# Performance work log

Measured on AMD Instinct MI355X. Metric: run time of the kernel, lower is better.

## Reference

```python
import jax, jax.numpy as jnp
import numpy as np

B, N, D = 32, 4096, 256
NC, NTPC, NVPT, NS = 16, 8, 4, 16
NT = NC * NTPC          # 128 type codes
NV = NT * NVPT          # 512 variant codes
THRESH = 0.1            # code_sparsity


def setup_inputs() -> dict:
    key = jax.random.key(0)
    ks = jax.random.split(key, 24)
    rn = lambda k, s, sc=0.02: jax.random.normal(k, s, jnp.float32) * sc
    return {
        "X": jax.random.normal(ks[0], (B, N, D), jnp.float32),
        "positions": jax.random.normal(ks[1], (B, N, D), jnp.float32),
        "mask": jnp.ones((B, N), jnp.bool_),
        "category_codes": rn(ks[2], (NC, D)),
        "type_codes": rn(ks[3], (NT, D)),
        "variant_codes": rn(ks[4], (NV, D)),
        "spatial_codes": rn(ks[5], (NS, D)),
        "log_tau": jnp.zeros((1,), jnp.float32),
        "Wk": rn(ks[6], (D, D)), "bk": jnp.zeros((D,), jnp.float32),
        "Wcat": rn(ks[7], (D, D)), "bcat": jnp.zeros((D,), jnp.float32),
        "Wtype": rn(ks[8], (D, D)), "btype": jnp.zeros((D,), jnp.float32),
        "Wvar": rn(ks[9], (D, D)), "bvar": jnp.zeros((D,), jnp.float32),
        "Wsp": rn(ks[10], (D, D)), "bsp": jnp.zeros((D,), jnp.float32),
        "Wg1": rn(ks[11], (D, 2 * D)), "bg1": jnp.zeros((D,), jnp.float32),
        "Wg2": rn(ks[12], (D, D)), "bg2": jnp.zeros((D,), jnp.float32),
        "Wo": rn(ks[13], (D, D)), "bo": jnp.zeros((D,), jnp.float32),
        "ln_g": jnp.ones((D,), jnp.float32), "ln_b": jnp.zeros((D,), jnp.float32),
        "level_weights": jnp.ones((4,), jnp.float32) / 4.0,
    }


def _sparsify(w, thr):
    w = jnp.where(w > thr, w, 0.0)
    return w / (w.sum(-1, keepdims=True) + 1e-8)


def reference(X, positions, mask, category_codes, type_codes, variant_codes,
              spatial_codes, log_tau, Wk, bk, Wcat, bcat, Wtype, btype,
              Wvar, bvar, Wsp, bsp, Wg1, bg1, Wg2, bg2, Wo, bo, ln_g, ln_b,
              level_weights):
    d = X.shape[-1]
    tau = jnp.clip(jnp.exp(log_tau) + 0.1, 0.1, 2.0)  # (1,)
    mv = jnp.finfo(X.dtype).min / 2
    K = X @ Wk.T + bk  # (B,N,d)

    def level(codes, Wq, bq):
        Q = codes @ Wq.T + bq                                    # (M,d)
        attn = jnp.einsum('md,bnd->bmn', Q, K) / jnp.sqrt(jnp.float32(d))
        attn = jnp.where(mask[:, None, :], attn, mv)
        attn = jnp.clip(attn, -50.0, 50.0)
        G = jnp.nan_to_num(jax.nn.softmax(attn, axis=-1))
        H = jnp.einsum('bmn,bnd->bmd', G, X)                     # (B,M,d)
        w_raw = jnp.linalg.norm(H, axis=-1) / tau                # (B,M)
        return H, w_raw

    # level 0: category
    H_cat, w_cat_raw = level(category_codes, Wcat, bcat)
    w_cat_sparse = _sparsify(jax.nn.softmax(w_cat_raw, -1), THRESH)
    # level 1: type (gated by category)
    H_type, w_type_raw = level(type_codes, Wtype, btype)
    w_type_g = (w_type_raw.reshape(-1, NC, NTPC) * w_cat_sparse[:, :, None]).reshape(-1, NT)
    w_type_sparse = _sparsify(jax.nn.softmax(w_type_g, -1), THRESH / 2)
    # level 2: variant (gated by type)
    H_var, w_var_raw = level(variant_codes, Wvar, bvar)
    w_type_exp = jnp.repeat(w_type_sparse, NVPT, axis=-1)        # (B,NV)
    w_var_sparse = _sparsify(jax.nn.softmax(w_var_raw * w_type_exp, -1), THRESH / 4)
    # spatial (independent)
    H_sp, w_sp_raw = level(spatial_codes, Wsp, bsp)
    w_sp_sparse = _sparsify(jax.nn.softmax(w_sp_raw, -1), THRESH)

    z_cat = jnp.einsum('bm,bmd->bd', w_cat_sparse, H_cat)
    z_type = jnp.einsum('bm,bmd->bd', w_type_sparse, H_type)
    z_var = jnp.einsum('bm,bmd->bd', w_var_sparse, H_var)
    z_sp = jnp.einsum('bm,bmd->bd', w_sp_sparse, H_sp)

    lw = jax.nn.softmax(level_weights)
    z = lw[0] * z_cat + lw[1] * z_type + lw[2] * z_var + lw[3] * z_sp

    # position gate: masked mean-pooled positions -> sigmoid gate
    m = mask.astype(X.dtype)
    pos_pool = (positions * m[:, :, None]).sum(1) / (m.sum(1, keepdims=True) + 1e-8)
    h = jax.nn.gelu(jnp.concatenate([z, pos_pool], -1) @ Wg1.T + bg1, approximate=False)
    gate = jax.nn.sigmoid(h @ Wg2.T + bg2)
    z = z * gate

    # out_proj: Linear + LayerNorm
    y = z @ Wo.T + bo
    mu = y.mean(-1, keepdims=True)
    var = ((y - mu) ** 2).mean(-1, keepdims=True)
    y = (y - mu) / jnp.sqrt(var + 1e-5) * ln_g + ln_b
    return y
```

## Files before the change

### kernel.cpp

```cpp
#include <hip/hip_runtime.h>

typedef unsigned short u16;
typedef short v8s __attribute__((ext_vector_type(8)));
typedef float v4f __attribute__((ext_vector_type(4)));

union U16x8 { uint4 u4; v8s s8; u16 us[8]; };

__device__ __forceinline__ u16 f2bf(float x) {
  unsigned int u = __float_as_uint(x);
  u += 0x7fffu + ((u >> 16) & 1u);
  return (u16)(u >> 16);
}

#define GLOBAL_AS __attribute__((address_space(1)))
#define LDS_AS __attribute__((address_space(3)))
__device__ __forceinline__ void async16(const void* g, void* l) {
  __builtin_amdgcn_global_load_lds((const GLOBAL_AS unsigned int*)g,
                                   (LDS_AS unsigned int*)l, 16, 0, 0);
}

#define BB 32
#define NN 4096
#define DD 256
#define M_TOT 672
#define M_PAD 704
#define CHUNK_B 16

__global__ void kz_zero(float* __restrict__ p, int n) {
  int i = blockIdx.x * 256 + threadIdx.x;
  if (i < n) p[i] = 0.f;
}

__global__ void k0_q(const float* __restrict__ cat, const float* __restrict__ typ,
                     const float* __restrict__ var, const float* __restrict__ spc,
                     const float* __restrict__ Wcat, const float* __restrict__ bcat,
                     const float* __restrict__ Wtype, const float* __restrict__ btype,
                     const float* __restrict__ Wvar, const float* __restrict__ bvar,
                     const float* __restrict__ Wsp, const float* __restrict__ bsp,
                     float* __restrict__ Qall) {
  __shared__ float cl[DD];
  const int m = blockIdx.x, tid = threadIdx.x;
  const float* codes = nullptr; const float* W = nullptr; const float* bia = nullptr; int r = 0;
  if (m < 16)       { codes = cat; r = m;       W = Wcat;  bia = bcat; }
  else if (m < 144) { codes = typ; r = m - 16;  W = Wtype; bia = btype; }
  else if (m < 656) { codes = var; r = m - 144; W = Wvar;  bia = bvar; }
  else if (m < 672) { codes = spc; r = m - 656; W = Wsp;   bia = bsp; }
  cl[tid] = (m < M_TOT) ? codes[r * DD + tid] : 0.f;
  __syncthreads();
  if (m < M_TOT) {
    float acc = bia[tid];
    const float4* w4 = (const float4*)(W + (size_t)tid * DD);
    const float4* c4 = (const float4*)cl;
    #pragma unroll 8
    for (int k = 0; k < 64; ++k) {
      float4 a = c4[k], b = w4[k];
      acc += a.x * b.x + a.y * b.y + a.z * b.z + a.w * b.w;
    }
    Qall[m * DD + tid] = acc;
  } else {
    Qall[m * DD + tid] = 0.f;
  }
}

__global__ void k1_qp(const float* __restrict__ Qall, const float* __restrict__ Wk,
                      const float* __restrict__ bk, u16* __restrict__ Qp,
                      float* __restrict__ qbw) {
  __shared__ float ql[DD];
  __shared__ float red[4];
  const int m = blockIdx.x, tid = threadIdx.x;
  ql[tid] = Qall[m * DD + tid];
  __syncthreads();
  float acc = 0.f;
  for (int j = 0; j < DD; ++j) acc += ql[j] * Wk[(size_t)j * DD + tid];
  Qp[m * DD + tid] = f2bf(acc);
  float p = ql[tid] * bk[tid];
  #pragma unroll
  for (int off = 32; off > 0; off >>= 1) p += __shfl_down(p, off, 64);
  if ((tid & 63) == 0) red[tid >> 6] = p;
  __syncthreads();
  if (tid == 0) qbw[m] = red[0] + red[1] + red[2] + red[3];
}

__global__ void k2_cast(const float* __restrict__ X, u16* __restrict__ Xb,
                        u16* __restrict__ XbT) {
  __shared__ u16 tl[64][72];
  const int n0 = blockIdx.x * 64, d0 = blockIdx.y * 64, b = blockIdx.z;
  const int tid = threadIdx.x;
  const int nl = tid >> 4, d4 = tid & 15;
  #pragma unroll
  for (int rr = 0; rr < 4; ++rr) {
    const int n = n0 + nl + rr * 16;
    float4 v = *(const float4*)(X + ((size_t)b * NN + n) * DD + d0 + d4 * 4);
    ushort4 h;
    h.x = f2bf(v.x); h.y = f2bf(v.y); h.z = f2bf(v.z); h.w = f2bf(v.w);
    *(ushort4*)(Xb + ((size_t)b * NN + n) * DD + d0 + d4 * 4) = h;
    *(ushort4*)(&tl[nl + rr * 16][d4 * 4]) = h;
  }
  __syncthreads();
  const int dl = tid >> 4, n4 = tid & 15;
  #pragma unroll
  for (int rr = 0; rr < 4; ++rr) {
    const int d = dl + rr * 16;
    ushort4 h;
    h.x = tl[n4 * 4 + 0][d]; h.y = tl[n4 * 4 + 1][d];
    h.z = tl[n4 * 4 + 2][d]; h.w = tl[n4 * 4 + 3][d];
    *(ushort4*)(XbT + ((size_t)b * DD + d0 + d) * NN + n0 + n4 * 4) = h;
  }
}

__global__ __launch_bounds__(256, 2) void p1_scores(
    const u16* __restrict__ Xb, const u16* __restrict__ Qp,
    const float* __restrict__ qbw, const unsigned char* __restrict__ mask,
    u16* __restrict__ P, float* __restrict__ sums, int b0) {
  __shared__ u16 sA[128 * 64];
  __shared__ u16 sB[128 * 64];
  const int tid = threadIdx.x;
  const int lane = tid & 63, w = tid >> 6;
  const int q = lane >> 4, c16 = lane & 15;
  const int n0 = blockIdx.x * 128, m0 = blockIdx.y * 128;
  const int b = b0 + blockIdx.z;
  const int wm = (w >> 1) * 64, wn = (w & 1) * 64;

  float qv[4][4];
  unsigned char mk[4];
  #pragma unroll
  for (int mi = 0; mi < 4; ++mi)
    #pragma unroll
    for (int r = 0; r < 4; ++r) {
      int row = m0 + wm + mi * 16 + q * 4 + r;
      qv[mi][r] = qbw[row < M_PAD ? row : M_PAD - 1];
    }
  #pragma unroll
  for (int ni = 0; ni < 4; ++ni)
    mk[ni] = mask[(size_t)b * NN + n0 + wn + ni * 16 + c16];

  v4f acc[4][4];
  #pragma unroll
  for (int mi = 0; mi < 4; ++mi)
    #pragma unroll
    for (int ni = 0; ni < 4; ++ni) acc[mi][ni] = (v4f){0.f, 0.f, 0.f, 0.f};

  const u16* Xbase = Xb + (size_t)b * NN * DD;
  for (int ks = 0; ks < 4; ++ks) {
    __syncthreads();
    #pragma unroll
    for (int i = 0; i < 4; ++i) {
      const int c = i * 256 + tid;
      const int row = c >> 3, kc = (c & 7) * 8;
      int gm = m0 + row; gm = gm < M_PAD ? gm : M_PAD - 1;
      async16(Qp + (size_t)gm * DD + ks * 64 + kc, sA + c * 8);
      async16(Xbase + (size_t)(n0 + row) * DD + ks * 64 + kc, sB + c * 8);
    }
    __syncthreads();
    #pragma unroll
    for (int kk = 0; kk < 2; ++kk) {
      v8s af[4], bf[4];
      #pragma unroll
      for (int mi = 0; mi < 4; ++mi) {
        U16x8 u; u.u4 = *(const uint4*)(sA + (wm + mi * 16 + c16) * 64 + kk * 32 + q * 8);
        af[mi] = u.s8;
      }
      #pragma unroll
      for (int ni = 0; ni < 4; ++ni) {
        U16x8 u; u.u4 = *(const uint4*)(sB + (wn + ni * 16 + c16) * 64 + kk * 32 + q * 8);
        bf[ni] = u.s8;
      }
      #pragma unroll
      for (int mi = 0; mi < 4; ++mi)
        #pragma unroll
        for (int ni = 0; ni < 4; ++ni)
          acc[mi][ni] = __builtin_amdgcn_mfma_f32_16x16x32_bf16(af[mi], bf[ni], acc[mi][ni], 0, 0, 0);
    }
  }

  float rs[4][4];
  #pragma unroll
  for (int mi = 0; mi < 4; ++mi)
    #pragma unroll
    for (int r = 0; r < 4; ++r) rs[mi][r] = 0.f;

  #pragma unroll
  for (int mi = 0; mi < 4; ++mi) {
    #pragma unroll
    for (int ni = 0; ni < 4; ++ni) {
      #pragma unroll
      for (int r = 0; r < 4; ++r) {
        float s = (acc[mi][ni][r] + qv[mi][r]) * 0.0625f;
        s = fminf(fmaxf(s, -50.f), 50.f);
        s = mk[ni] ? s : -50.f;
        float p = __expf(s);
        rs[mi][r] += p;
        const int row = m0 + wm + mi * 16 + q * 4 + r;
        if (row < M_TOT)
          P[((size_t)(b - b0) * M_TOT + row) * NN + n0 + wn + ni * 16 + c16] = f2bf(p);
      }
    }
  }
  #pragma unroll
  for (int mi = 0; mi < 4; ++mi) {
    #pragma unroll
    for (int r = 0; r < 4; ++r) {
      float v = rs[mi][r];
      v += __shfl_xor(v, 1, 64);
      v += __shfl_xor(v, 2, 64);
      v += __shfl_xor(v, 4, 64);
      v += __shfl_xor(v, 8, 64);
      const int row = m0 + wm + mi * 16 + q * 4 + r;
      if (c16 == 0 && row < M_TOT)
        atomicAdd(&sums[(size_t)b * M_PAD + row], v);
    }
  }
}

__global__ __launch_bounds__(256, 4) void p2_h(
    const u16* __restrict__ P, const u16* __restrict__ XbT,
    const float* __restrict__ sums, float* __restrict__ Hws,
    float* __restrict__ nrm, int b0) {
  __shared__ u16 sA[64 * 64];
  __shared__ u16 sB[128 * 64];
  const int tid = threadIdx.x;
  const int lane = tid & 63, w = tid >> 6;
  const int q = lane >> 4, c16 = lane & 15;
  const int d0 = blockIdx.x * 128, m0 = blockIdx.y * 64;
  const int b = b0 + blockIdx.z;
  const int wm = (w >> 1) * 32, wd = (w & 1) * 64;

  v4f acc[2][4];
  #pragma unroll
  for (int mi = 0; mi < 2; ++mi)
    #pragma unroll
    for (int ni = 0; ni < 4; ++ni) acc[mi][ni] = (v4f){0.f, 0.f, 0.f, 0.f};

  const u16* Pb = P + (size_t)(b - b0) * M_TOT * NN;
  const u16* Tb = XbT + ((size_t)b * DD + d0) * NN;

  for (int ks = 0; ks < NN / 64; ++ks) {
    __syncthreads();
    #pragma unroll
    for (int i = 0; i < 2; ++i) {
      const int c = i * 256 + tid;
      const int row = c >> 3, kc = (c & 7) * 8;
      int gm = m0 + row; gm = gm < M_TOT ? gm : M_TOT - 1;
      async16(Pb + (size_t)gm * NN + ks * 64 + kc, sA + c * 8);
    }
    #pragma unroll
    for (int i = 0; i < 4; ++i) {
      const int c = i * 256 + tid;
      const int row = c >> 3, kc = (c & 7) * 8;
      async16(Tb + (size_t)row * NN + ks * 64 + kc, sB + c * 8);
    }
    __syncthreads();
    #pragma unroll
    for (int kk = 0; kk < 2; ++kk) {
      v8s af[2], bf[4];
      #pragma unroll
      for (int mi = 0; mi < 2; ++mi) {
        U16x8 u; u.u4 = *(const uint4*)(sA + (wm + mi * 16 + c16) * 64 + kk * 32 + q * 8);
        af[mi] = u.s8;
      }
      #pragma unroll
      for (int ni = 0; ni < 4; ++ni) {
        U16x8 u; u.u4 = *(const uint4*)(sB + (wd + ni * 16 + c16) * 64 + kk * 32 + q * 8);
        bf[ni] = u.s8;
      }
      #pragma unroll
      for (int mi = 0; mi < 2; ++mi)
        #pragma unroll
        for (int ni = 0; ni < 4; ++ni)
          acc[mi][ni] = __builtin_amdgcn_mfma_f32_16x16x32_bf16(af[mi], bf[ni], acc[mi][ni], 0, 0, 0);
    }
  }

  float sv[2][4], ns[2][4];
  #pragma unroll
  for (int mi = 0; mi < 2; ++mi)
    #pragma unroll
    for (int r = 0; r < 4; ++r) {
      const int row = m0 + wm + mi * 16 + q * 4 + r;
      sv[mi][r] = sums[(size_t)b * M_PAD + row];
      ns[mi][r] = 0.f;
    }
  #pragma unroll
  for (int mi = 0; mi < 2; ++mi) {
    #pragma unroll
    for (int ni = 0; ni < 4; ++ni) {
      #pragma unroll
      for (int r = 0; r < 4; ++r) {
        const int row = m0 + wm + mi * 16 + q * 4 + r;
        float h = acc[mi][ni][r] / sv[mi][r];
        ns[mi][r] += h * h;
        Hws[((size_t)b * M_PAD + row) * DD + d0 + wd + ni * 16 + c16] = h;
      }
    }
  }
  #pragma unroll
  for (int mi = 0; mi < 2; ++mi) {
    #pragma unroll
    for (int r = 0; r < 4; ++r) {
      float v = ns[mi][r];
      v += __shfl_xor(v, 1, 64);
      v += __shfl_xor(v, 2, 64);
      v += __shfl_xor(v, 4, 64);
      v += __shfl_xor(v, 8, 64);
      const int row = m0 + wm + mi * 16 + q * 4 + r;
      if (c16 == 0 && row < M_TOT)
        atomicAdd(&nrm[(size_t)b * M_PAD + row], v);
    }
  }
}

__global__ void k4_pool(const float* __restrict__ pos, const unsigned char* __restrict__ mask,
                        float* __restrict__ pp, float* __restrict__ cnt) {
  __shared__ float sp[4][256];
  __shared__ float sc[4];
  const int cx = blockIdx.x, b = blockIdx.y, tid = threadIdx.x;
  const int nl = tid >> 6, d4 = tid & 63;
  const int n0 = cx * 256;
  float4 acc = {0.f, 0.f, 0.f, 0.f};
  float c = 0.f;
  for (int i = 0; i < 64; ++i) {
    const int n = n0 + i * 4 + nl;
    const float m = mask[(size_t)b * NN + n] ? 1.f : 0.f;
    c += m;
    float4 v = *(const float4*)(pos + ((size_t)b * NN + n) * DD + d4 * 4);
    acc.x += m * v.x; acc.y += m * v.y; acc.z += m * v.z; acc.w += m * v.w;
  }
  *(float4*)(&sp[nl][d4 * 4]) = acc;
  if (d4 == 0) sc[nl] = c;
  __syncthreads();
  pp[((size_t)b * 16 + cx) * DD + tid] = sp[0][tid] + sp[1][tid] + sp[2][tid] + sp[3][tid];
  if (tid == 0) cnt[b * 16 + cx] = sc[0] + sc[1] + sc[2] + sc[3];
}

__device__ void softmax_sparsify(const float* in, int nn, float* outp, float thr) {
  float mx = -3.4e38f;
  for (int i = 0; i < nn; ++i) mx = fmaxf(mx, in[i]);
  float s = 0.f;
  for (int i = 0; i < nn; ++i) { float e = __expf(in[i] - mx); outp[i] = e; s += e; }
  float s2 = 0.f;
  for (int i = 0; i < nn; ++i) {
    float v = outp[i] / s;
    v = (v > thr) ? v : 0.f;
    outp[i] = v; s2 += v;
  }
  const float inv = 1.f / (s2 + 1e-8f);
  for (int i = 0; i < nn; ++i) outp[i] *= inv;
}

__global__ void k5_final(const float* __restrict__ Hws, const float* __restrict__ nrm,
                         const float* __restrict__ pp, const float* __restrict__ cnt,
                         const float* __restrict__ log_tau,
                         const float* __restrict__ Wg1, const float* __restrict__ bg1,
                         const float* __restrict__ Wg2, const float* __restrict__ bg2,
                         const float* __restrict__ Wo, const float* __restrict__ bo,
                         const float* __restrict__ lng, const float* __restrict__ lnb,
                         const float* __restrict__ lvlw, float* __restrict__ out) {
  __shared__ float wr[M_TOT];
  __shared__ float wcat[16], wtyp[128], wvar[512], wsp[16], lw[4];
  __shared__ float wbuf[M_TOT];
  __shared__ float zpart[4][DD];
  __shared__ float zb[DD], pb[DD], hb[DD], zg[DD];
  __shared__ float red[8];
  const int b = blockIdx.x, tid = threadIdx.x;
  const int lane = tid & 63, w = tid >> 6;
  const float tau = fminf(fmaxf(__expf(log_tau[0]) + 0.1f, 0.1f), 2.0f);
  const float* Hb = Hws + (size_t)b * M_PAD * DD;

  for (int m = tid; m < M_TOT; m += 256)
    wr[m] = sqrtf(nrm[(size_t)b * M_PAD + m]) / tau;
  __syncthreads();

  if (tid == 0) {
    softmax_sparsify(wr, 16, wcat, 0.1f);
    for (int i = 0; i < 128; ++i) wbuf[i] = wr[16 + i] * wcat[i >> 3];
    softmax_sparsify(wbuf, 128, wtyp, 0.05f);
    for (int i = 0; i < 512; ++i) wvar[i] = wr[144 + i] * wtyp[i >> 2];
    softmax_sparsify(wvar, 512, wvar, 0.025f);
    softmax_sparsify(wr + 656, 16, wsp, 0.1f);
    float mx = fmaxf(fmaxf(lvlw[0], lvlw[1]), fmaxf(lvlw[2], lvlw[3]));
    float s = 0.f;
    for (int i = 0; i < 4; ++i) { lw[i] = __expf(lvlw[i] - mx); s += lw[i]; }
    for (int i = 0; i < 4; ++i) lw[i] /= s;
  }
  __syncthreads();

  for (int m = tid; m < M_TOT; m += 256) {
    float v;
    if (m < 16)       v = lw[0] * wcat[m];
    else if (m < 144) v = lw[1] * wtyp[m - 16];
    else if (m < 656) v = lw[2] * wvar[m - 144];
    else              v = lw[3] * wsp[m - 656];
    wbuf[m] = v;
  }
  __syncthreads();

  {
    float4 zp = {0.f, 0.f, 0.f, 0.f};
    for (int m = w; m < M_TOT; m += 4) {
      const float wv = wbuf[m];
      float4 hv = *(const float4*)(Hb + (size_t)m * DD + lane * 4);
      zp.x += wv * hv.x; zp.y += wv * hv.y; zp.z += wv * hv.z; zp.w += wv * hv.w;
    }
    *(float4*)(&zpart[w][lane * 4]) = zp;
  }
  __syncthreads();
  float z = zpart[0][tid] + zpart[1][tid] + zpart[2][tid] + zpart[3][tid];
  float p = 0.f, c = 0.f;
  for (int ch = 0; ch < 16; ++ch) {
    p += pp[((size_t)b * 16 + ch) * DD + tid];
    c += cnt[b * 16 + ch];
  }
  p /= (c + 1e-8f);
  zb[tid] = z; pb[tid] = p;
  __syncthreads();

  float h = bg1[tid];
  {
    const float4* w4 = (const float4*)(Wg1 + (size_t)tid * 512);
    const float4* z4 = (const float4*)zb;
    const float4* p4 = (const float4*)pb;
    for (int k = 0; k < 64; ++k) {
      float4 a = z4[k], bb = w4[k];
      h += a.x * bb.x + a.y * bb.y + a.z * bb.z + a.w * bb.w;
    }
    for (int k = 0; k < 64; ++k) {
      float4 a = p4[k], bb = w4[64 + k];
      h += a.x * bb.x + a.y * bb.y + a.z * bb.z + a.w * bb.w;
    }
  }
  h = 0.5f * h * (1.f + erff(h * 0.70710678118654752f));
  hb[tid] = h;
  __syncthreads();

  float g = bg2[tid];
  {
    const float4* w4 = (const float4*)(Wg2 + (size_t)tid * DD);
    const float4* h4 = (const float4*)hb;
    for (int k = 0; k < 64; ++k) {
      float4 a = h4[k], bb = w4[k];
      g += a.x * bb.x + a.y * bb.y + a.z * bb.z + a.w * bb.w;
    }
  }
  g = 1.f / (1.f + __expf(-g));
  zg[tid] = zb[tid] * g;
  __syncthreads();

  float y = bo[tid];
  {
    const float4* w4 = (const float4*)(Wo + (size_t)tid * DD);
    const float4* z4 = (const float4*)zg;
    for (int k = 0; k < 64; ++k) {
      float4 a = z4[k], bb = w4[k];
      y += a.x * bb.x + a.y * bb.y + a.z * bb.z + a.w * bb.w;
    }
  }

  float s = y;
  #pragma unroll
  for (int off = 32; off > 0; off >>= 1) s += __shfl_xor(s, off, 64);
  if (lane == 0) red[w] = s;
  __syncthreads();
  const float mu = (red[0] + red[1] + red[2] + red[3]) * (1.f / 256.f);
  float dv = (y - mu) * (y - mu);
  #pragma unroll
  for (int off = 32; off > 0; off >>= 1) dv += __shfl_xor(dv, off, 64);
  if (lane == 0) red[4 + w] = dv;
  __syncthreads();
  const float var = (red[4] + red[5] + red[6] + red[7]) * (1.f / 256.f);
  out[(size_t)b * DD + tid] = (y - mu) / sqrtf(var + 1e-5f) * lng[tid] + lnb[tid];
}

extern "C" void kernel_launch(void* const* d_in, const int* in_sizes, int n_in,
                              void* d_out, int out_size, void* d_ws, size_t ws_size,
                              hipStream_t stream) {
  const float* X          = (const float*)d_in[0];
  const float* positions  = (const float*)d_in[1];
  const unsigned char* mask = (const unsigned char*)d_in[2];
  const float* cat  = (const float*)d_in[3];
  const float* typ  = (const float*)d_in[4];
  const float* var  = (const float*)d_in[5];
  const float* spc  = (const float*)d_in[6];
  const float* log_tau = (const float*)d_in[7];
  const float* Wk   = (const float*)d_in[8];   const float* bk    = (const float*)d_in[9];
  const float* Wcat = (const float*)d_in[10];  const float* bcat  = (const float*)d_in[11];
  const float* Wtype= (const float*)d_in[12];  const float* btype = (const float*)d_in[13];
  const float* Wvar = (const float*)d_in[14];  const float* bvar  = (const float*)d_in[15];
  const float* Wsp  = (const float*)d_in[16];  const float* bsp   = (const float*)d_in[17];
  const float* Wg1  = (const float*)d_in[18];  const float* bg1   = (const float*)d_in[19];
  const float* Wg2  = (const float*)d_in[20];  const float* bg2   = (const float*)d_in[21];
  const float* Wo   = (const float*)d_in[22];  const float* bo    = (const float*)d_in[23];
  const float* lng  = (const float*)d_in[24];  const float* lnb   = (const float*)d_in[25];
  const float* lvlw = (const float*)d_in[26];

  char* ws = (char*)d_ws;
  const size_t oXb   = 0;
  const size_t oXT   = oXb + 67108864;
  const size_t oP    = oXT + 67108864;
  const size_t oQall = oP + 88080384;
  const size_t oQp   = oQall + 720896;
  const size_t oQb   = oQp + 360448;
  const size_t oSums = oQb + 2816;
  const size_t oNrm  = oSums + 90112;
  const size_t oH    = oNrm + 90112;
  const size_t oPP   = oH + 23068672;
  const size_t oCNT  = oPP + 524288;

  u16*   Xb   = (u16*)(ws + oXb);
  u16*   XbT  = (u16*)(ws + oXT);
  u16*   P    = (u16*)(ws + oP);
  float* Qall = (float*)(ws + oQall);
  u16*   Qp   = (u16*)(ws + oQp);
  float* qbw  = (float*)(ws + oQb);
  float* sums = (float*)(ws + oSums);
  float* nrm  = (float*)(ws + oNrm);
  float* Hws  = (float*)(ws + oH);
  float* ppw  = (float*)(ws + oPP);
  float* cntw = (float*)(ws + oCNT);

  kz_zero<<<(2 * BB * M_PAD + 255) / 256, 256, 0, stream>>>(sums, 2 * BB * M_PAD);
  k0_q<<<M_PAD, 256, 0, stream>>>(cat, typ, var, spc, Wcat, bcat, Wtype, btype,
                                  Wvar, bvar, Wsp, bsp, Qall);
  k1_qp<<<M_PAD, 256, 0, stream>>>(Qall, Wk, bk, Qp, qbw);
  k2_cast<<<dim3(64, 4, 32), 256, 0, stream>>>(X, Xb, XbT);
  k4_pool<<<dim3(16, 32), 256, 0, stream>>>(positions, mask, ppw, cntw);
  for (int chunk = 0; chunk < 2; ++chunk) {
    const int b0 = chunk * CHUNK_B;
    p1_scores<<<dim3(32, 6, CHUNK_B), 256, 0, stream>>>(Xb, Qp, qbw, mask, P, sums, b0);
    p2_h<<<dim3(2, 11, CHUNK_B), 256, 0, stream>>>(P, XbT, sums, Hws, nrm, b0);
  }
  k5_final<<<32, 256, 0, stream>>>(Hws, nrm, ppw, cntw, log_tau, Wg1, bg1, Wg2, bg2,
                                   Wo, bo, lng, lnb, lvlw, (float*)d_out);
}
```

Before: 850.1 us.

## Split final kernel into weights/z-reduction/MLP and run scores in one chunk when workspace allows

The single 32-block final kernel is split into three kernels. The code weights are computed and stored globally, the weighted sum over H is spread across 8x32 blocks with atomicAdd into a zeroed accumulator, and the gate MLP and LayerNorm run in a separate kernel. The workspace layout is now computed at runtime, so the score/H passes can run as one chunk over all 32 batches when the workspace is large enough, which removes a pair of launches and serialisation. This adds two kernel launches and a non-deterministic atomic summation order.

```diff
diff --git a/kernel.cpp b/kernel.cpp
--- a/kernel.cpp
+++ b/kernel.cpp
@@ -24,7 +24,6 @@
 #define DD 256
 #define M_TOT 672
 #define M_PAD 704
-#define CHUNK_B 16
 
 __global__ void kz_zero(float* __restrict__ p, int n) {
   int i = blockIdx.x * 256 + threadIdx.x;
@@ -347,33 +346,20 @@
   for (int i = 0; i < nn; ++i) outp[i] *= inv;
 }
 
-__global__ void k5_final(const float* __restrict__ Hws, const float* __restrict__ nrm,
-                         const float* __restrict__ pp, const float* __restrict__ cnt,
-                         const float* __restrict__ log_tau,
-                         const float* __restrict__ Wg1, const float* __restrict__ bg1,
-                         const float* __restrict__ Wg2, const float* __restrict__ bg2,
-                         const float* __restrict__ Wo, const float* __restrict__ bo,
-                         const float* __restrict__ lng, const float* __restrict__ lnb,
-                         const float* __restrict__ lvlw, float* __restrict__ out) {
+__global__ void k5a_weights(const float* __restrict__ nrm, const float* __restrict__ log_tau,
+                            const float* __restrict__ lvlw, float* __restrict__ wbufG) {
   __shared__ float wr[M_TOT];
   __shared__ float wcat[16], wtyp[128], wvar[512], wsp[16], lw[4];
-  __shared__ float wbuf[M_TOT];
-  __shared__ float zpart[4][DD];
-  __shared__ float zb[DD], pb[DD], hb[DD], zg[DD];
-  __shared__ float red[8];
+  __shared__ float tmp[128];
   const int b = blockIdx.x, tid = threadIdx.x;
-  const int lane = tid & 63, w = tid >> 6;
   const float tau = fminf(fmaxf(__expf(log_tau[0]) + 0.1f, 0.1f), 2.0f);
-  const float* Hb = Hws + (size_t)b * M_PAD * DD;
-
   for (int m = tid; m < M_TOT; m += 256)
     wr[m] = sqrtf(nrm[(size_t)b * M_PAD + m]) / tau;
   __syncthreads();
-
   if (tid == 0) {
     softmax_sparsify(wr, 16, wcat, 0.1f);
-    for (int i = 0; i < 128; ++i) wbuf[i] = wr[16 + i] * wcat[i >> 3];
-    softmax_sparsify(wbuf, 128, wtyp, 0.05f);
+    for (int i = 0; i < 128; ++i) tmp[i] = wr[16 + i] * wcat[i >> 3];
+    softmax_sparsify(tmp, 128, wtyp, 0.05f);
     for (int i = 0; i < 512; ++i) wvar[i] = wr[144 + i] * wtyp[i >> 2];
     softmax_sparsify(wvar, 512, wvar, 0.025f);
     softmax_sparsify(wr + 656, 16, wsp, 0.1f);
@@ -383,35 +369,49 @@
     for (int i = 0; i < 4; ++i) lw[i] /= s;
   }
   __syncthreads();
-
   for (int m = tid; m < M_TOT; m += 256) {
     float v;
     if (m < 16)       v = lw[0] * wcat[m];
     else if (m < 144) v = lw[1] * wtyp[m - 16];
     else if (m < 656) v = lw[2] * wvar[m - 144];
     else              v = lw[3] * wsp[m - 656];
-    wbuf[m] = v;
-  }
-  __syncthreads();
-
-  {
-    float4 zp = {0.f, 0.f, 0.f, 0.f};
-    for (int m = w; m < M_TOT; m += 4) {
-      const float wv = wbuf[m];
-      float4 hv = *(const float4*)(Hb + (size_t)m * DD + lane * 4);
-      zp.x += wv * hv.x; zp.y += wv * hv.y; zp.z += wv * hv.z; zp.w += wv * hv.w;
-    }
-    *(float4*)(&zpart[w][lane * 4]) = zp;
-  }
-  __syncthreads();
-  float z = zpart[0][tid] + zpart[1][tid] + zpart[2][tid] + zpart[3][tid];
+    wbufG[(size_t)b * M_PAD + m] = v;
+  }
+}
+
+__global__ void k5b_z(const float* __restrict__ Hws, const float* __restrict__ wbufG,
+                      float* __restrict__ zacc) {
+  const int mc = blockIdx.x, b = blockIdx.y, tid = threadIdx.x;
+  const float* Hb = Hws + (size_t)b * M_PAD * DD;
+  const float* wb = wbufG + (size_t)b * M_PAD;
+  float acc = 0.f;
+  #pragma unroll 4
+  for (int i = 0; i < 84; ++i) {
+    const int m = mc * 84 + i;
+    acc += wb[m] * Hb[(size_t)m * DD + tid];
+  }
+  atomicAdd(&zacc[(size_t)b * DD + tid], acc);
+}
+
+__global__ void k5c_mlp(const float* __restrict__ zacc, const float* __restrict__ pp,
+                        const float* __restrict__ cnt,
+                        const float* __restrict__ Wg1, const float* __restrict__ bg1,
+                        const float* __restrict__ Wg2, const float* __restrict__ bg2,
+                        const float* __restrict__ Wo, const float* __restrict__ bo,
+                        const float* __restrict__ lng, const float* __restrict__ lnb,
+                        float* __restrict__ out) {
+  __shared__ float zb[DD], pb[DD], hb[DD], zg[DD];
+  __shared__ float red[8];
+  const int b = blockIdx.x, tid = threadIdx.x;
+  const int lane = tid & 63, w = tid >> 6;
+
   float p = 0.f, c = 0.f;
   for (int ch = 0; ch < 16; ++ch) {
     p += pp[((size_t)b * 16 + ch) * DD + tid];
     c += cnt[b * 16 + ch];
   }
-  p /= (c + 1e-8f);
-  zb[tid] = z; pb[tid] = p;
+  zb[tid] = zacc[(size_t)b * DD + tid];
+  pb[tid] = p / (c + 1e-8f);
   __syncthreads();
 
   float h = bg1[tid];
@@ -493,41 +493,54 @@
   const float* lvlw = (const float*)d_in[26];
 
   char* ws = (char*)d_ws;
-  const size_t oXb   = 0;
-  const size_t oXT   = oXb + 67108864;
-  const size_t oP    = oXT + 67108864;
-  const size_t oQall = oP + 88080384;
-  const size_t oQp   = oQall + 720896;
-  const size_t oQb   = oQp + 360448;
-  const size_t oSums = oQb + 2816;
-  const size_t oNrm  = oSums + 90112;
-  const size_t oH    = oNrm + 90112;
-  const size_t oPP   = oH + 23068672;
-  const size_t oCNT  = oPP + 524288;
+  size_t off = 0;
+  auto alloc = [&](size_t bytes) { size_t o = off; off = (off + bytes + 255) & ~255ULL; return o; };
+  const size_t oXb   = alloc((size_t)BB * NN * DD * 2);
+  const size_t oXT   = alloc((size_t)BB * DD * NN * 2);
+  const size_t oQall = alloc((size_t)M_PAD * DD * 4);
+  const size_t oQp   = alloc((size_t)M_PAD * DD * 2);
+  const size_t oQb   = alloc((size_t)M_PAD * 4);
+  const size_t oSums = alloc((size_t)BB * M_PAD * 4);
+  const size_t oNrm  = alloc((size_t)BB * M_PAD * 4);
+  const size_t oZac  = alloc((size_t)BB * DD * 4);
+  const size_t oWbf  = alloc((size_t)BB * M_PAD * 4);
+  const size_t oH    = alloc((size_t)BB * M_PAD * DD * 4);
+  const size_t oPP   = alloc((size_t)BB * 16 * DD * 4);
+  const size_t oCNT  = alloc((size_t)BB * 16 * 4);
+  const size_t oP    = alloc(0);
+
+  const size_t pFull = (size_t)BB * M_TOT * NN * 2;
+  const int chunks  = (ws_size >= oP + pFull) ? 1 : 2;
+  const int chunkB  = BB / chunks;
 
   u16*   Xb   = (u16*)(ws + oXb);
   u16*   XbT  = (u16*)(ws + oXT);
-  u16*   P    = (u16*)(ws + oP);
   float* Qall = (float*)(ws + oQall);
   u16*   Qp   = (u16*)(ws + oQp);
   float* qbw  = (float*)(ws + oQb);
   float* sums = (float*)(ws + oSums);
   float* nrm  = (float*)(ws + oNrm);
+  float* zacc = (float*)(ws + oZac);
+  float* wbfG = (float*)(ws + oWbf);
   float* Hws  = (float*)(ws + oH);
   float* ppw  = (float*)(ws + oPP);
   float* cntw = (float*)(ws + oCNT);
-
-  kz_zero<<<(2 * BB * M_PAD + 255) / 256, 256, 0, stream>>>(sums, 2 * BB * M_PAD);
+  u16*   P    = (u16*)(ws + oP);
+
+  const int nzero = 2 * BB * M_PAD + BB * DD;
+  kz_zero<<<(nzero + 255) / 256, 256, 0, stream>>>(sums, nzero);
   k0_q<<<M_PAD, 256, 0, stream>>>(cat, typ, var, spc, Wcat, bcat, Wtype, btype,
                                   Wvar, bvar, Wsp, bsp, Qall);
   k1_qp<<<M_PAD, 256, 0, stream>>>(Qall, Wk, bk, Qp, qbw);
   k2_cast<<<dim3(64, 4, 32), 256, 0, stream>>>(X, Xb, XbT);
   k4_pool<<<dim3(16, 32), 256, 0, stream>>>(positions, mask, ppw, cntw);
-  for (int chunk = 0; chunk < 2; ++chunk) {
-    const int b0 = chunk * CHUNK_B;
-    p1_scores<<<dim3(32, 6, CHUNK_B), 256, 0, stream>>>(Xb, Qp, qbw, mask, P, sums, b0);
-    p2_h<<<dim3(2, 11, CHUNK_B), 256, 0, stream>>>(P, XbT, sums, Hws, nrm, b0);
-  }
-  k5_final<<<32, 256, 0, stream>>>(Hws, nrm, ppw, cntw, log_tau, Wg1, bg1, Wg2, bg2,
-                                   Wo, bo, lng, lnb, lvlw, (float*)d_out);
-}
+  for (int chunk = 0; chunk < chunks; ++chunk) {
+    const int b0 = chunk * chunkB;
+    p1_scores<<<dim3(32, 6, chunkB), 256, 0, stream>>>(Xb, Qp, qbw, mask, P, sums, b0);
+    p2_h<<<dim3(2, 11, chunkB), 256, 0, stream>>>(P, XbT, sums, Hws, nrm, b0);
+  }
+  k5a_weights<<<32, 256, 0, stream>>>(nrm, log_tau, lvlw, wbfG);
+  k5b_z<<<dim3(8, 32), 256, 0, stream>>>(Hws, wbfG, zacc);
+  k5c_mlp<<<32, 256, 0, stream>>>(zacc, ppw, cntw, Wg1, bg1, Wg2, bg2, Wo, bo,
+                                  lng, lnb, (float*)d_out);
+}
```

Result: faster. 750.1 us (-11.8%).
